# Kernel optimization log

Measured on AMD Instinct MI355X. Metric: run time of the kernel, lower is better.

## Reference

```python
import jax, jax.numpy as jnp
import numpy as np

N_NODES = 50000
N_FEAT = 128
N_EDGES = 800000
HEADS1 = 4
HID1 = 64
HID2 = 128
N_CLASSES = 10
N_GRAPHS = 512
NEG_SLOPE_ATT = 0.2   # GATConv attention leaky relu
NEG_SLOPE_ACT = 0.01  # F.leaky_relu default between layers


def setup_inputs() -> dict:
    key = jax.random.key(0)
    ks = jax.random.split(key, 20)
    s = 0.05
    inp = {
        'x': jax.random.normal(ks[0], (N_NODES, N_FEAT), dtype=jnp.float32),
        'edge_index': jax.random.randint(ks[1], (2, N_EDGES), 0, N_NODES, dtype=jnp.int64),
        'edge_attr': jax.random.normal(ks[2], (N_EDGES, 8), dtype=jnp.float32),
        'batch': jnp.sort(jax.random.randint(ks[3], (N_NODES,), 0, N_GRAPHS, dtype=jnp.int64)),
        # conv1: F -> HID1, heads=4, concat
        'W1': jax.random.normal(ks[4], (N_FEAT, HEADS1 * HID1), dtype=jnp.float32) * s,
        'a_src1': jax.random.normal(ks[5], (HEADS1, HID1), dtype=jnp.float32) * s,
        'a_dst1': jax.random.normal(ks[6], (HEADS1, HID1), dtype=jnp.float32) * s,
        'b1': jnp.zeros((HEADS1 * HID1,), dtype=jnp.float32),
        # conv2: 4*HID1 -> HID2, heads=1
        'W2': jax.random.normal(ks[7], (HEADS1 * HID1, HID2), dtype=jnp.float32) * s,
        'a_src2': jax.random.normal(ks[8], (1, HID2), dtype=jnp.float32) * s,
        'a_dst2': jax.random.normal(ks[9], (1, HID2), dtype=jnp.float32) * s,
        'b2': jnp.zeros((HID2,), dtype=jnp.float32),
        # conv3: HID2 -> N_CLASSES, heads=1
        'W3': jax.random.normal(ks[10], (HID2, N_CLASSES), dtype=jnp.float32) * s,
        'a_src3': jax.random.normal(ks[11], (1, N_CLASSES), dtype=jnp.float32) * s,
        'a_dst3': jax.random.normal(ks[12], (1, N_CLASSES), dtype=jnp.float32) * s,
        'b3': jnp.zeros((N_CLASSES,), dtype=jnp.float32),
    }
    return inp


def gat_conv(x, src, dst, W, a_src, a_dst, b, n_nodes, heads, ch):
    """PyG GATConv (concat=True, add_self_loops already applied in src/dst)."""
    h = (x @ W).reshape(n_nodes, heads, ch)            # [N,H,C]
    al_s = (h * a_src).sum(-1)                          # [N,H]
    al_d = (h * a_dst).sum(-1)                          # [N,H]
    e = jax.nn.leaky_relu(al_s[src] + al_d[dst], NEG_SLOPE_ATT)  # [E,H]
    # segment softmax over incoming edges per destination node
    m = jax.ops.segment_max(e, dst, num_segments=n_nodes)
    ex = jnp.exp(e - m[dst])
    den = jax.ops.segment_sum(ex, dst, num_segments=n_nodes)
    alpha = ex / (den[dst] + 1e-16)                     # [E,H]
    out = jax.ops.segment_sum(h[src] * alpha[..., None], dst, num_segments=n_nodes)
    return out.reshape(n_nodes, heads * ch) + b


def reference(x, edge_index, edge_attr, batch,
              W1, a_src1, a_dst1, b1,
              W2, a_src2, a_dst2, b2,
              W3, a_src3, a_dst3, b3):
    # GATConv adds self-loops by default; edge_attr unused (edge_dim=None)
    loops = jnp.arange(N_NODES, dtype=edge_index.dtype)
    src = jnp.concatenate([edge_index[0], loops])
    dst = jnp.concatenate([edge_index[1], loops])

    h = gat_conv(x, src, dst, W1, a_src1, a_dst1, b1, N_NODES, HEADS1, HID1)
    h = jax.nn.leaky_relu(h, NEG_SLOPE_ACT)
    h = gat_conv(h, src, dst, W2, a_src2, a_dst2, b2, N_NODES, 1, HID2)
    h = jax.nn.leaky_relu(h, NEG_SLOPE_ACT)
    h = gat_conv(h, src, dst, W3, a_src3, a_dst3, b3, N_NODES, 1, N_CLASSES)

    pooled = jax.ops.segment_sum(h, batch, num_segments=N_GRAPHS)  # global_add_pool
    return jax.nn.log_softmax(pooled, axis=1), pooled
```

## Files before the change

### kernel.cpp

```cpp
#include <hip/hip_runtime.h>
#include <math.h>

#define NNODES 50000
#define MPAD   50048
#define NFEAT  128
#define NEDGE  800000
#define ETOT   (NEDGE + NNODES)
#define H1     4
#define O1     256
#define C2     128
#define C3     10
#define NGRAPH 512

#define NBKT   196
#define NBLK1  831
#define EPB    1024
#define SCM    (NBKT * NBLK1)
#define SCB    637

typedef __attribute__((ext_vector_type(8))) short short8;
typedef __attribute__((ext_vector_type(4))) float f32x4;

__device__ __forceinline__ unsigned short f2b(float f) {
  unsigned int u = __float_as_uint(f);
  u += 0x7fffu + ((u >> 16) & 1u);
  return (unsigned short)(u >> 16);
}
__device__ __forceinline__ float b2f(unsigned short u) {
  return __uint_as_float(((unsigned int)u) << 16);
}
__device__ __forceinline__ float readlane_f(float v, int l) {
  return __uint_as_float((unsigned)__builtin_amdgcn_readlane(__float_as_uint(v), l));
}


__global__ void k_prep(const float* __restrict__ W1, const float* __restrict__ as1,
                       const float* __restrict__ ad1,
                       float* __restrict__ was, float* __restrict__ wad) {
  int tid = threadIdx.x;
  int h = tid >> 7, k = tid & 127;
  float s = 0.f, d = 0.f;
  for (int j = 0; j < 64; ++j) {
    float w = W1[(size_t)k * 256 + h * 64 + j];
    s += w * as1[h * 64 + j];
    d += w * ad1[h * 64 + j];
  }
  was[h * 128 + k] = s;
  wad[h * 128 + k] = d;
}

#define NB_CVT 12500

__global__ __launch_bounds__(256) void k_front(
    const int* __restrict__ src_e, const int* __restrict__ dst_e,
    int* __restrict__ hists,
    const float* __restrict__ X, unsigned short* __restrict__ Xb,
    const float* __restrict__ W1,
    const float* __restrict__ was, const float* __restrict__ wad,
    float* __restrict__ als, float* __restrict__ ald,
    unsigned short* __restrict__ W1p,
    const float* __restrict__ W2, unsigned short* __restrict__ W2p,
    const float* __restrict__ W3, unsigned short* __restrict__ W3p) {
  const int b = blockIdx.x;
  const int tid = threadIdx.x;
  if (b < NBLK1) {
    __shared__ int h[NBKT];
    if (tid < NBKT) h[tid] = 0;
    __syncthreads();
    const int base = b * EPB;
#pragma unroll
    for (int r = 0; r < 4; ++r) {
      int e = base + r * 256 + tid;
      if (e < ETOT) {
        int d = (e < NEDGE) ? dst_e[e] : (e - NEDGE);
        atomicAdd(&h[d >> 8], 1);
      }
    }
    __syncthreads();
    if (tid < NBKT) hists[tid * NBLK1 + b] = h[tid];
  } else if (b < NBLK1 + NB_CVT) {
    const int n = (b - NBLK1) * 4 + (tid >> 6);
    const int lane = tid & 63;
    const int k0 = lane * 2;
    float2 xv = *(const float2*)(X + (size_t)n * 128 + k0);
    ushort2 o; o.x = f2b(xv.x); o.y = f2b(xv.y);
    *(ushort2*)(Xb + (size_t)n * 128 + k0) = o;
    float s[4], d[4];
#pragma unroll
    for (int h = 0; h < 4; ++h) {
      float2 wsv = *(const float2*)(was + h * 128 + k0);
      float2 wdv = *(const float2*)(wad + h * 128 + k0);
      s[h] = xv.x * wsv.x + xv.y * wsv.y;
      d[h] = xv.x * wdv.x + xv.y * wdv.y;
    }
#pragma unroll
    for (int m = 1; m < 64; m <<= 1)
#pragma unroll
      for (int h = 0; h < 4; ++h) { s[h] += __shfl_xor(s[h], m); d[h] += __shfl_xor(d[h], m); }
    if (lane == 0) {
#pragma unroll
      for (int h = 0; h < 4; ++h) {
        als[(size_t)n * 4 + h] = s[h];
        ald[(size_t)n * 4 + h] = d[h];
      }
    }
  } else if (b < NBLK1 + NB_CVT + 128) {
    int idx = (b - NBLK1 - NB_CVT) * 256 + tid;
    int h = idx >> 13, r = idx & 8191;
    int j = r & 7, lane = (r >> 3) & 63, t = r >> 9;
    int ks = t & 3, nt = t >> 2;
    int k = ks * 32 + (lane >> 4) * 8 + j;
    int n = nt * 16 + (lane & 15);
    W1p[idx] = f2b(W1[(size_t)k * 256 + h * 64 + n]);
  } else if (b < NBLK1 + NB_CVT + 256) {
    int idx = (b - NBLK1 - NB_CVT - 128) * 256 + tid;
    int j = idx & 7, lane = (idx >> 3) & 63, t = idx >> 9;
    int ks = t % 8, nt = t / 8;
    int k = ks * 32 + (lane >> 4) * 8 + j;
    int n = nt * 16 + (lane & 15);
    W2p[idx] = f2b(W2[(size_t)k * C2 + n]);
  } else {
    int idx = (b - NBLK1 - NB_CVT - 256) * 256 + tid;
    int j = idx & 7, lane = (idx >> 3) & 63, t = idx >> 9;
    int ks = t & 3, nt = t >> 2;
    int k = ks * 32 + (lane >> 4) * 8 + j;
    int n = nt * 16 + (lane & 15);
    W3p[idx] = f2b((n < C3) ? W3[(size_t)k * C3 + n] : 0.f);
  }
}


__global__ __launch_bounds__(256) void k_scanA2(const int* __restrict__ a,
                                                int* __restrict__ bsum) {
  int idx = blockIdx.x * 256 + threadIdx.x;
  int v = (idx < SCM) ? a[idx] : 0;
#pragma unroll
  for (int m = 1; m < 64; m <<= 1) v += __shfl_xor(v, m);
  __shared__ int ws[4];
  int lane = threadIdx.x & 63, wid = threadIdx.x >> 6;
  if (lane == 0) ws[wid] = v;
  __syncthreads();
  if (threadIdx.x == 0) bsum[blockIdx.x] = ws[0] + ws[1] + ws[2] + ws[3];
}

__global__ __launch_bounds__(256) void k_scanMid(int* __restrict__ bsum) {
  __shared__ int ws[4];
  __shared__ int carry_s;
  const int tid = threadIdx.x, lane = tid & 63, wid = tid >> 6;
  if (tid == 0) carry_s = 0;
  __syncthreads();
  for (int base = 0; base < SCB; base += 256) {
    int j = base + tid;
    int v = (j < SCB) ? bsum[j] : 0;
    int s = v;
#pragma unroll
    for (int m = 1; m < 64; m <<= 1) {
      int t = __shfl_up(s, m);
      if (lane >= m) s += t;
    }
    if (lane == 63) ws[wid] = s;
    __syncthreads();
    int woff = 0;
#pragma unroll
    for (int k = 0; k < 4; ++k)
      if (k < wid) woff += ws[k];
    int c = carry_s;
    int tot = ws[0] + ws[1] + ws[2] + ws[3];
    if (j < SCB) bsum[j] = c + woff + s - v;
    __syncthreads();
    if (tid == 0) carry_s = c + tot;
    __syncthreads();
  }
}

__global__ __launch_bounds__(256) void k_scanB2(int* __restrict__ a,
                                                const int* __restrict__ bsum,
                                                int* __restrict__ cb) {
  const int b = blockIdx.x, tid = threadIdx.x;
  const int lane = tid & 63, wid = tid >> 6;
  __shared__ int ws[4];
  int idx = b * 256 + tid;
  int v = (idx < SCM) ? a[idx] : 0;
  int s = v;
#pragma unroll
  for (int m = 1; m < 64; m <<= 1) {
    int t = __shfl_up(s, m);
    if (lane >= m) s += t;
  }
  if (lane == 63) ws[wid] = s;
  __syncthreads();
  int woff = 0;
#pragma unroll
  for (int k = 0; k < 4; ++k)
    if (k < wid) woff += ws[k];
  int excl = bsum[b] + woff + s - v;
  if (idx < SCM) {
    a[idx] = excl;
    if (idx % NBLK1 == 0) cb[idx / NBLK1] = excl;
  }
  if (b == 0 && tid == 0) cb[NBKT] = ETOT;
}


__global__ __launch_bounds__(256) void k_part1(const int* __restrict__ src_e,
                                               const int* __restrict__ dst_e,
                                               const int* __restrict__ offs,
                                               unsigned* __restrict__ coarse) {
  __shared__ int cur[NBKT];
  const int b = blockIdx.x;
  const int tid = threadIdx.x;
  if (tid < NBKT) cur[tid] = offs[tid * NBLK1 + b];
  __syncthreads();
  const int base = b * EPB;
#pragma unroll
  for (int r = 0; r < 4; ++r) {
    int e = base + r * 256 + tid;
    if (e < ETOT) {
      int d, s;
      if (e < NEDGE) { d = dst_e[e]; s = src_e[e]; }
      else           { d = e - NEDGE; s = e - NEDGE; }
      int pos = atomicAdd(&cur[d >> 8], 1);
      coarse[pos] = ((unsigned)d << 16) | (unsigned)s;
    }
  }
}


__global__ __launch_bounds__(256) void k_bucket(const unsigned* __restrict__ coarse,
                                                const int* __restrict__ cb,
                                                int* __restrict__ rowptr,
                                                int* __restrict__ srcs) {
  const int b = blockIdx.x;
  const int tid = threadIdx.x;
  const int lane = tid & 63, wid = tid >> 6;
  const int lo = cb[b], hi = cb[b + 1];
  __shared__ int h[256];
  __shared__ int cur[256];
  __shared__ int ws[4];
  h[tid] = 0;
  __syncthreads();
  for (int i = lo + tid; i < hi; i += 256)
    atomicAdd(&h[(coarse[i] >> 16) & 255], 1);
  __syncthreads();
  int v = h[tid];
  int s = v;
#pragma unroll
  for (int m = 1; m < 64; m <<= 1) {
    int t = __shfl_up(s, m);
    if (lane >= m) s += t;
  }
  if (lane == 63) ws[wid] = s;
  __syncthreads();
  int woff = 0;
#pragma unroll
  for (int k = 0; k < 4; ++k)
    if (k < wid) woff += ws[k];
  int ex = woff + s - v;
  cur[tid] = lo + ex;
  int d = b * 256 + tid;
  if (d < NNODES) rowptr[d] = lo + ex;
  if (b == NBKT - 1 && tid == 0) rowptr[NNODES] = ETOT;
  __syncthreads();
  for (int i = lo + tid; i < hi; i += 256) {
    unsigned c = coarse[i];
    int pos = atomicAdd(&cur[(c >> 16) & 255], 1);
    srcs[pos] = (int)(c & 0xffffu);
  }
}


__global__ __launch_bounds__(512) void k_aggP(const int* __restrict__ rowptr,
                                              const int* __restrict__ srcs,
                                              const unsigned short* __restrict__ Xb,
                                              const float* __restrict__ als,
                                              const float* __restrict__ ald,
                                              unsigned short* __restrict__ P) {
  __shared__ float exs[8][16][4];
  const int wv = threadIdx.x >> 6;
  const int n = blockIdx.x * 8 + wv;
  const int lane = threadIdx.x & 63;
  const int r0 = rowptr[n], r1 = rowptr[n + 1];
  const int e_lane = lane & 15, hh = lane >> 4;
  const float aldv = ald[(size_t)n * 4 + hh];
  const int ch0 = lane * 2;
  float a00 = 0.f, a01 = 0.f, a10 = 0.f, a11 = 0.f;
  float a20 = 0.f, a21 = 0.f, a30 = 0.f, a31 = 0.f;
  float den = 0.f;
  for (int i0 = r0; i0 < r1; i0 += 16) {
    const int take = r1 - i0;
    int sidx = srcs[min(i0 + e_lane, r1 - 1)];
    float ev = als[(size_t)sidx * 4 + hh] + aldv;
    ev = (ev > 0.f) ? ev : 0.2f * ev;
    float exv = (e_lane < take) ? __expf(ev) : 0.f;
    den += exv;
    exs[wv][e_lane][hh] = exv;
    unsigned hv[16];
#pragma unroll
    for (int m = 0; m < 16; ++m) {
      int s = __builtin_amdgcn_readlane(sidx, m);
      hv[m] = *(const unsigned*)(Xb + (size_t)s * 128 + ch0);
    }
#pragma unroll
    for (int m = 0; m < 16; ++m) {
      float4 e4 = *(const float4*)(&exs[wv][m][0]);
      float x0 = __uint_as_float(hv[m] << 16);
      float x1 = __uint_as_float(hv[m] & 0xffff0000u);
      a00 += e4.x * x0; a01 += e4.x * x1;
      a10 += e4.y * x0; a11 += e4.y * x1;
      a20 += e4.z * x0; a21 += e4.z * x1;
      a30 += e4.w * x0; a31 += e4.w * x1;
    }
  }
#pragma unroll
  for (int m = 1; m < 16; m <<= 1) den += __shfl_xor(den, m);
  float acc[4][2] = {{a00,a01},{a10,a11},{a20,a21},{a30,a31}};
#pragma unroll
  for (int h = 0; h < 4; ++h) {
    float rd = 1.f / (readlane_f(den, h * 16) + 1e-16f);
    ushort2 o; o.x = f2b(acc[h][0] * rd); o.y = f2b(acc[h][1] * rd);
    *(ushort2*)(P + ((size_t)n * 4 + h) * 128 + ch0) = o;
  }
}


__global__ __launch_bounds__(256) void k_mmh(const unsigned short* __restrict__ P,
                                             const unsigned short* __restrict__ Wp,
                                             const float* __restrict__ b1,
                                             unsigned short* __restrict__ act1) {
  const int hy = blockIdx.y;
  const int w = threadIdx.x >> 6, lane = threadIdx.x & 63;
  const int arow = blockIdx.x * 64 + w * 16 + (lane & 15);
  const int k0 = (lane >> 4) * 8;
  const unsigned short* Ab = P + ((size_t)arow * 4 + hy) * 128;
  f32x4 acc[4] = {};
#pragma unroll
  for (int ks = 0; ks < 4; ++ks) {
    short8 a = *(const short8*)(Ab + ks * 32 + k0);
    const short8* bp = (const short8*)(Wp + (size_t)hy * 8192) + ks * 64 + lane;
#pragma unroll
    for (int nt = 0; nt < 4; ++nt) {
      short8 b = bp[(size_t)nt * 4 * 64];
      acc[nt] = __builtin_amdgcn_mfma_f32_16x16x32_bf16(a, b, acc[nt], 0, 0, 0);
    }
  }
  const int col = lane & 15;
  const int rbase = blockIdx.x * 64 + w * 16 + (lane >> 4) * 4;
#pragma unroll
  for (int nt = 0; nt < 4; ++nt) {
    int ch = hy * 64 + nt * 16 + col;
    float bb = b1[ch];
#pragma unroll
    for (int j = 0; j < 4; ++j) {
      float v = acc[nt][j] + bb;
      v = (v > 0.f) ? v : 0.01f * v;
      act1[(size_t)(rbase + j) * 256 + ch] = f2b(v);
    }
  }
}


template<int K, int N, int HEADS, int CREAL>
__global__ __launch_bounds__(256) void k_mm(const unsigned short* __restrict__ Xb,
                                            const unsigned short* __restrict__ Wp,
                                            unsigned short* __restrict__ Hout,
                                            const float* __restrict__ a_src,
                                            const float* __restrict__ a_dst,
                                            float* __restrict__ als,
                                            float* __restrict__ ald) {
  constexpr int KS = K / 32, NT = N / 16;
  constexpr int NTH = (NT + HEADS - 1) / HEADS;
  const int w = threadIdx.x >> 6, lane = threadIdx.x & 63;
  const int arow = blockIdx.x * 64 + w * 16 + (lane & 15);
  const int k0 = (lane >> 4) * 8;
  f32x4 acc[NT] = {};
  for (int ks = 0; ks < KS; ++ks) {
    short8 a = *(const short8*)(Xb + (size_t)arow * K + ks * 32 + k0);
    const short8* bp = (const short8*)Wp + (size_t)ks * 64 + lane;
#pragma unroll
    for (int nt = 0; nt < NT; ++nt) {
      short8 b = bp[(size_t)nt * KS * 64];
      acc[nt] = __builtin_amdgcn_mfma_f32_16x16x32_bf16(a, b, acc[nt], 0, 0, 0);
    }
  }
  const int col = lane & 15;
  const int rbase = blockIdx.x * 64 + w * 16 + (lane >> 4) * 4;
#pragma unroll
  for (int nt = 0; nt < NT; ++nt)
#pragma unroll
    for (int j = 0; j < 4; ++j)
      Hout[(size_t)(rbase + j) * N + nt * 16 + col] = f2b(acc[nt][j]);

  float av[NT], dv[NT];
#pragma unroll
  for (int nt = 0; nt < NT; ++nt) {
    int ch = nt * 16 + col;
    av[nt] = (ch < CREAL) ? a_src[ch] : 0.f;
    dv[nt] = (ch < CREAL) ? a_dst[ch] : 0.f;
  }
  float sa[HEADS][4], da[HEADS][4];
#pragma unroll
  for (int h = 0; h < HEADS; ++h)
#pragma unroll
    for (int j = 0; j < 4; ++j) { sa[h][j] = 0.f; da[h][j] = 0.f; }
#pragma unroll
  for (int nt = 0; nt < NT; ++nt) {
    int h = nt / NTH;
#pragma unroll
    for (int j = 0; j < 4; ++j) {
      sa[h][j] += acc[nt][j] * av[nt];
      da[h][j] += acc[nt][j] * dv[nt];
    }
  }
#pragma unroll
  for (int mask = 1; mask < 16; mask <<= 1)
#pragma unroll
    for (int h = 0; h < HEADS; ++h)
#pragma unroll
      for (int j = 0; j < 4; ++j) {
        sa[h][j] += __shfl_xor(sa[h][j], mask);
        da[h][j] += __shfl_xor(da[h][j], mask);
      }
  if (col == 0) {
#pragma unroll
    for (int j = 0; j < 4; ++j)
#pragma unroll
      for (int h = 0; h < HEADS; ++h) {
        als[(size_t)(rbase + j) * HEADS + h] = sa[h][j];
        ald[(size_t)(rbase + j) * HEADS + h] = da[h][j];
      }
  }
}


template<int C, bool ACT>
__global__ __launch_bounds__(512) void k_agg(const int* __restrict__ rowptr,
                                             const int* __restrict__ srcs,
                                             const unsigned short* __restrict__ Hm,
                                             const float* __restrict__ als,
                                             const float* __restrict__ ald,
                                             const float* __restrict__ bias,
                                             unsigned short* __restrict__ outb) {
  const int n = blockIdx.x * 8 + (threadIdx.x >> 6);
  const int lane = threadIdx.x & 63;
  const int r0 = rowptr[n], r1 = rowptr[n + 1];
  const int e_lane = lane & 15;
  const int ch0 = lane * 2;
  const float aldm = ald[n];
  float acc0 = 0.f, acc1 = 0.f, den = 0.f;
  for (int i0 = r0; i0 < r1; i0 += 16) {
    const int take = r1 - i0;
    int sidx = srcs[min(i0 + e_lane, r1 - 1)];
    float ev = als[sidx] + aldm;
    ev = (ev > 0.f) ? ev : 0.2f * ev;
    float exv = (lane < 16 && e_lane < take) ? __expf(ev) : 0.f;
    den += exv;
    unsigned hv[16];
#pragma unroll
    for (int m = 0; m < 16; ++m) {
      int s = __builtin_amdgcn_readlane(sidx, m);
      hv[m] = *(const unsigned*)(Hm + (size_t)s * C + ch0);
    }
#pragma unroll
    for (int m = 0; m < 16; ++m) {
      float ex = readlane_f(exv, m);
      acc0 += ex * __uint_as_float(hv[m] << 16);
      acc1 += ex * __uint_as_float(hv[m] & 0xffff0000u);
    }
  }
#pragma unroll
  for (int mask = 1; mask < 64; mask <<= 1) den += __shfl_xor(den, mask);
  float rden = 1.f / (den + 1e-16f);
  float v0 = acc0 * rden + bias[ch0];
  float v1 = acc1 * rden + bias[ch0 + 1];
  if (ACT) { v0 = (v0 > 0.f) ? v0 : 0.01f * v0; v1 = (v1 > 0.f) ? v1 : 0.01f * v1; }
  ushort2 o; o.x = f2b(v0); o.y = f2b(v1);
  *(ushort2*)(outb + (size_t)n * C + ch0) = o;
}


__global__ __launch_bounds__(512) void k_agg3(const int* __restrict__ rowptr,
                                              const int* __restrict__ srcs,
                                              const unsigned short* __restrict__ Hm,
                                              const float* __restrict__ als,
                                              const float* __restrict__ ald,
                                              const float* __restrict__ bias,
                                              float* __restrict__ pooled,
                                              const int* __restrict__ batch) {
  const int n = blockIdx.x * 8 + (threadIdx.x >> 6);
  const int lane = threadIdx.x & 63;
  const int r0 = rowptr[n], r1 = rowptr[n + 1];
  const int e_lane = lane & 15;
  const float aldm = ald[n];
  float acc = 0.f, den = 0.f;
  for (int i0 = r0; i0 < r1; i0 += 16) {
    const int take = r1 - i0;
    int sidx = srcs[min(i0 + e_lane, r1 - 1)];
    float ev = als[sidx] + aldm;
    ev = (ev > 0.f) ? ev : 0.2f * ev;
    float exv = (lane < 16 && e_lane < take) ? __expf(ev) : 0.f;
    den += exv;
    unsigned short hs[16];
#pragma unroll
    for (int m = 0; m < 16; ++m) {
      int s = __builtin_amdgcn_readlane(sidx, m);
      hs[m] = Hm[(size_t)s * 16 + e_lane];
    }
#pragma unroll
    for (int m = 0; m < 16; ++m) {
      float ex = readlane_f(exv, m);
      acc += ex * b2f(hs[m]);
    }
  }
#pragma unroll
  for (int mask = 1; mask < 64; mask <<= 1) den += __shfl_xor(den, mask);
  if (lane < C3) {
    float val = acc / (den + 1e-16f) + bias[lane];
    atomicAdd(&pooled[(size_t)batch[n] * C3 + lane], val);
  }
}


__global__ void k_lsm(const float* __restrict__ pooled, float* __restrict__ dout) {
  int g = blockIdx.x * 256 + threadIdx.x;
  if (g >= NGRAPH) return;
  float v[C3];
  float mx = -1e30f;
#pragma unroll
  for (int c = 0; c < C3; ++c) { v[c] = pooled[g * C3 + c]; mx = fmaxf(mx, v[c]); }
  float ssum = 0.f;
#pragma unroll
  for (int c = 0; c < C3; ++c) ssum += __expf(v[c] - mx);
  float lse = mx + __logf(ssum);
#pragma unroll
  for (int c = 0; c < C3; ++c) {
    dout[g * C3 + c] = v[c] - lse;
    dout[NGRAPH * C3 + g * C3 + c] = v[c];
  }
}


extern "C" void kernel_launch(void* const* d_in, const int* in_sizes, int n_in,
                              void* d_out, int out_size, void* d_ws, size_t ws_size,
                              hipStream_t stream) {
  (void)in_sizes; (void)n_in; (void)out_size; (void)ws_size;
  const float* x     = (const float*)d_in[0];
  const int*   eix   = (const int*)d_in[1];
  const int*   batch = (const int*)d_in[3];
  const float* W1 = (const float*)d_in[4];
  const float* as1 = (const float*)d_in[5];
  const float* ad1 = (const float*)d_in[6];
  const float* b1 = (const float*)d_in[7];
  const float* W2 = (const float*)d_in[8];
  const float* as2 = (const float*)d_in[9];
  const float* ad2 = (const float*)d_in[10];
  const float* b2 = (const float*)d_in[11];
  const float* W3 = (const float*)d_in[12];
  const float* as3 = (const float*)d_in[13];
  const float* ad3 = (const float*)d_in[14];
  const float* b3 = (const float*)d_in[15];
  const int* src_e = eix;
  const int* dst_e = eix + NEDGE;

  char* ws = (char*)d_ws;
  size_t off = 0;
  auto carve = [&](size_t bytes) -> char* {
    char* p = ws + off;
    off += (bytes + 511) & ~(size_t)511;
    return p;
  };
  int* hists  = (int*)carve((size_t)SCM * 4);
  int* bsum   = (int*)carve((size_t)SCB * 4);
  int* cb     = (int*)carve((size_t)(NBKT + 1) * 4);
  unsigned* coarse = (unsigned*)carve((size_t)ETOT * 4);
  int* rowptr = (int*)carve((size_t)(NNODES + 1) * 4);
  int* srcs   = (int*)carve((size_t)ETOT * 4);
  float* als  = (float*)carve((size_t)MPAD * H1 * 4);
  float* ald  = (float*)carve((size_t)MPAD * H1 * 4);
  float* was  = (float*)carve((size_t)512 * 4);
  float* wad  = (float*)carve((size_t)512 * 4);
  unsigned short* Xb   = (unsigned short*)carve((size_t)MPAD * 128 * 2);
  unsigned short* P    = (unsigned short*)carve((size_t)MPAD * 512 * 2);
  unsigned short* act1 = (unsigned short*)carve((size_t)MPAD * 256 * 2);
  unsigned short* Hb   = (unsigned short*)carve((size_t)MPAD * 128 * 2);
  unsigned short* Xc   = (unsigned short*)carve((size_t)MPAD * 128 * 2);
  unsigned short* H3b  = (unsigned short*)carve((size_t)MPAD * 16 * 2);
  float* pooled = (float*)carve((size_t)NGRAPH * C3 * 4);
  unsigned short* W1p = (unsigned short*)carve((size_t)4 * 8192 * 2);
  unsigned short* W2p = (unsigned short*)carve((size_t)O1 * C2 * 2);
  unsigned short* W3p = (unsigned short*)carve((size_t)C2 * 16 * 2);

  hipMemsetAsync(pooled, 0, (size_t)NGRAPH * C3 * 4, stream);

  k_prep<<<1, 512, 0, stream>>>(W1, as1, ad1, was, wad);
  k_front<<<NBLK1 + NB_CVT + 264, 256, 0, stream>>>(
      src_e, dst_e, hists, x, Xb, W1, was, wad, als, ald, W1p, W2, W2p, W3, W3p);
  k_scanA2<<<SCB, 256, 0, stream>>>(hists, bsum);
  k_scanMid<<<1, 256, 0, stream>>>(bsum);
  k_scanB2<<<SCB, 256, 0, stream>>>(hists, bsum, cb);
  k_part1<<<NBLK1, 256, 0, stream>>>(src_e, dst_e, hists, coarse);
  k_bucket<<<NBKT, 256, 0, stream>>>(coarse, cb, rowptr, srcs);

  const int GB = MPAD / 64;
  const int NB8 = NNODES / 8;

  k_aggP<<<NB8, 512, 0, stream>>>(rowptr, srcs, Xb, als, ald, P);
  k_mmh<<<dim3(GB, 4), 256, 0, stream>>>(P, W1p, b1, act1);

  k_mm<O1, C2, 1, C2><<<GB, 256, 0, stream>>>(act1, W2p, Hb, as2, ad2, als, ald);
  k_agg<C2, true><<<NB8, 512, 0, stream>>>(rowptr, srcs, Hb, als, ald, b2, Xc);

  k_mm<C2, 16, 1, C3><<<GB, 256, 0, stream>>>(Xc, W3p, H3b, as3, ad3, als, ald);
  k_agg3<<<NB8, 512, 0, stream>>>(rowptr, srcs, H3b, als, ald, b3, pooled, batch);

  k_lsm<<<(NGRAPH + 255) / 256, 256, 0, stream>>>(pooled, (float*)d_out);
}
```

Baseline: 228.2 us.

## Use packed FP32 FMAs in aggregation and pack four nodes per wave in layer 3

The layer-1 and layer-2 aggregation inner loops now use v_pk_fma_f32 inline asm, with attention weights staged through shared memory, which roughly halves the FMA instruction count. The layer-3 aggregation kernel previously used only 16 of 64 lanes per wave. It now processes four destination nodes per wave in 16-lane groups, with per-group source indices and weights in LDS, and launches four times fewer blocks. This targets ALU issue cost and idle lanes, at the price of extra LDS traffic and no explicit barrier around the shared-memory reuse within a wave.

```diff
diff --git a/kernel.cpp b/kernel.cpp
--- a/kernel.cpp
+++ b/kernel.cpp
@@ -20,6 +20,7 @@
 
 typedef __attribute__((ext_vector_type(8))) short short8;
 typedef __attribute__((ext_vector_type(4))) float f32x4;
+typedef __attribute__((ext_vector_type(2))) float f32x2;
 
 __device__ __forceinline__ unsigned short f2b(float f) {
   unsigned int u = __float_as_uint(f);
@@ -283,8 +284,7 @@
   const int e_lane = lane & 15, hh = lane >> 4;
   const float aldv = ald[(size_t)n * 4 + hh];
   const int ch0 = lane * 2;
-  float a00 = 0.f, a01 = 0.f, a10 = 0.f, a11 = 0.f;
-  float a20 = 0.f, a21 = 0.f, a30 = 0.f, a31 = 0.f;
+  f32x2 ah0 = {0.f, 0.f}, ah1 = {0.f, 0.f}, ah2 = {0.f, 0.f}, ah3 = {0.f, 0.f};
   float den = 0.f;
   for (int i0 = r0; i0 < r1; i0 += 16) {
     const int take = r1 - i0;
@@ -302,18 +302,24 @@
     }
 #pragma unroll
     for (int m = 0; m < 16; ++m) {
-      float4 e4 = *(const float4*)(&exs[wv][m][0]);
-      float x0 = __uint_as_float(hv[m] << 16);
-      float x1 = __uint_as_float(hv[m] & 0xffff0000u);
-      a00 += e4.x * x0; a01 += e4.x * x1;
-      a10 += e4.y * x0; a11 += e4.y * x1;
-      a20 += e4.z * x0; a21 += e4.z * x1;
-      a30 += e4.w * x0; a31 += e4.w * x1;
+      f32x2 e01 = *(const f32x2*)(&exs[wv][m][0]);
+      f32x2 e23 = *(const f32x2*)(&exs[wv][m][2]);
+      f32x2 x2;
+      x2.x = __uint_as_float(hv[m] << 16);
+      x2.y = __uint_as_float(hv[m] & 0xffff0000u);
+      asm("v_pk_fma_f32 %0, %1, %2, %0 op_sel:[0,0,0] op_sel_hi:[1,0,1]"
+          : "+v"(ah0) : "v"(x2), "v"(e01));
+      asm("v_pk_fma_f32 %0, %1, %2, %0 op_sel:[0,1,0] op_sel_hi:[1,1,1]"
+          : "+v"(ah1) : "v"(x2), "v"(e01));
+      asm("v_pk_fma_f32 %0, %1, %2, %0 op_sel:[0,0,0] op_sel_hi:[1,0,1]"
+          : "+v"(ah2) : "v"(x2), "v"(e23));
+      asm("v_pk_fma_f32 %0, %1, %2, %0 op_sel:[0,1,0] op_sel_hi:[1,1,1]"
+          : "+v"(ah3) : "v"(x2), "v"(e23));
     }
   }
 #pragma unroll
   for (int m = 1; m < 16; m <<= 1) den += __shfl_xor(den, m);
-  float acc[4][2] = {{a00,a01},{a10,a11},{a20,a21},{a30,a31}};
+  float acc[4][2] = {{ah0.x, ah0.y}, {ah1.x, ah1.y}, {ah2.x, ah2.y}, {ah3.x, ah3.y}};
 #pragma unroll
   for (int h = 0; h < 4; ++h) {
     float rd = 1.f / (readlane_f(den, h * 16) + 1e-16f);
@@ -440,13 +446,16 @@
                                              const float* __restrict__ ald,
                                              const float* __restrict__ bias,
                                              unsigned short* __restrict__ outb) {
-  const int n = blockIdx.x * 8 + (threadIdx.x >> 6);
+  __shared__ float exs2[8][16];
+  const int wv = threadIdx.x >> 6;
+  const int n = blockIdx.x * 8 + wv;
   const int lane = threadIdx.x & 63;
   const int r0 = rowptr[n], r1 = rowptr[n + 1];
   const int e_lane = lane & 15;
   const int ch0 = lane * 2;
   const float aldm = ald[n];
-  float acc0 = 0.f, acc1 = 0.f, den = 0.f;
+  f32x2 accP0 = {0.f, 0.f}, accP1 = {0.f, 0.f};
+  float den = 0.f;
   for (int i0 = r0; i0 < r1; i0 += 16) {
     const int take = r1 - i0;
     int sidx = srcs[min(i0 + e_lane, r1 - 1)];
@@ -454,6 +463,7 @@
     ev = (ev > 0.f) ? ev : 0.2f * ev;
     float exv = (lane < 16 && e_lane < take) ? __expf(ev) : 0.f;
     den += exv;
+    if (lane < 16) exs2[wv][lane] = exv;
     unsigned hv[16];
 #pragma unroll
     for (int m = 0; m < 16; ++m) {
@@ -461,14 +471,21 @@
       hv[m] = *(const unsigned*)(Hm + (size_t)s * C + ch0);
     }
 #pragma unroll
-    for (int m = 0; m < 16; ++m) {
-      float ex = readlane_f(exv, m);
-      acc0 += ex * __uint_as_float(hv[m] << 16);
-      acc1 += ex * __uint_as_float(hv[m] & 0xffff0000u);
+    for (int m = 0; m < 16; m += 2) {
+      f32x2 ep = *(const f32x2*)(&exs2[wv][m]);
+      f32x2 xa, xb;
+      xa.x = __uint_as_float(hv[m] << 16);
+      xa.y = __uint_as_float(hv[m + 1] << 16);
+      xb.x = __uint_as_float(hv[m] & 0xffff0000u);
+      xb.y = __uint_as_float(hv[m + 1] & 0xffff0000u);
+      asm("v_pk_fma_f32 %0, %1, %2, %0" : "+v"(accP0) : "v"(ep), "v"(xa));
+      asm("v_pk_fma_f32 %0, %1, %2, %0" : "+v"(accP1) : "v"(ep), "v"(xb));
     }
   }
 #pragma unroll
   for (int mask = 1; mask < 64; mask <<= 1) den += __shfl_xor(den, mask);
+  float acc0 = accP0.x + accP0.y;
+  float acc1 = accP1.x + accP1.y;
   float rden = 1.f / (den + 1e-16f);
   float v0 = acc0 * rden + bias[ch0];
   float v1 = acc1 * rden + bias[ch0 + 1];
@@ -486,36 +503,38 @@
                                               const float* __restrict__ bias,
                                               float* __restrict__ pooled,
                                               const int* __restrict__ batch) {
-  const int n = blockIdx.x * 8 + (threadIdx.x >> 6);
+  __shared__ int   sid_s[8][4][16];
+  __shared__ float exv_s[8][4][16];
+  const int wv = threadIdx.x >> 6;
   const int lane = threadIdx.x & 63;
-  const int r0 = rowptr[n], r1 = rowptr[n + 1];
-  const int e_lane = lane & 15;
-  const float aldm = ald[n];
+  const int g = lane >> 4, el = lane & 15;
+  const int n = blockIdx.x * 32 + wv * 4 + g;
+  const bool valid = n < NNODES;
+  int r0 = 0, r1 = 0;
+  float aldm = 0.f;
+  if (valid) { r0 = rowptr[n]; r1 = rowptr[n + 1]; aldm = ald[n]; }
   float acc = 0.f, den = 0.f;
   for (int i0 = r0; i0 < r1; i0 += 16) {
     const int take = r1 - i0;
-    int sidx = srcs[min(i0 + e_lane, r1 - 1)];
+    int sidx = srcs[min(i0 + el, r1 - 1)];
     float ev = als[sidx] + aldm;
     ev = (ev > 0.f) ? ev : 0.2f * ev;
-    float exv = (lane < 16 && e_lane < take) ? __expf(ev) : 0.f;
+    float exv = (el < take) ? __expf(ev) : 0.f;
     den += exv;
-    unsigned short hs[16];
+    sid_s[wv][g][el] = sidx;
+    exv_s[wv][g][el] = exv;
 #pragma unroll
     for (int m = 0; m < 16; ++m) {
-      int s = __builtin_amdgcn_readlane(sidx, m);
-      hs[m] = Hm[(size_t)s * 16 + e_lane];
-    }
-#pragma unroll
-    for (int m = 0; m < 16; ++m) {
-      float ex = readlane_f(exv, m);
-      acc += ex * b2f(hs[m]);
-    }
-  }
-#pragma unroll
-  for (int mask = 1; mask < 64; mask <<= 1) den += __shfl_xor(den, mask);
-  if (lane < C3) {
-    float val = acc / (den + 1e-16f) + bias[lane];
-    atomicAdd(&pooled[(size_t)batch[n] * C3 + lane], val);
+      int s = sid_s[wv][g][m];
+      float ex = exv_s[wv][g][m];
+      acc += ex * b2f(Hm[(size_t)s * 16 + el]);
+    }
+  }
+#pragma unroll
+  for (int mask = 1; mask < 16; mask <<= 1) den += __shfl_xor(den, mask);
+  if (valid && el < C3) {
+    float val = acc / (den + 1e-16f) + bias[el];
+    atomicAdd(&pooled[(size_t)batch[n] * C3 + el], val);
   }
 }
 
@@ -602,6 +621,7 @@
 
   const int GB = MPAD / 64;
   const int NB8 = NNODES / 8;
+  const int NB32 = (NNODES + 31) / 32;
 
   k_aggP<<<NB8, 512, 0, stream>>>(rowptr, srcs, Xb, als, ald, P);
   k_mmh<<<dim3(GB, 4), 256, 0, stream>>>(P, W1p, b1, act1);
@@ -610,7 +630,7 @@
   k_agg<C2, true><<<NB8, 512, 0, stream>>>(rowptr, srcs, Hb, als, ald, b2, Xc);
 
   k_mm<C2, 16, 1, C3><<<GB, 256, 0, stream>>>(Xc, W3p, H3b, as3, ad3, als, ald);
-  k_agg3<<<NB8, 512, 0, stream>>>(rowptr, srcs, H3b, als, ald, b3, pooled, batch);
+  k_agg3<<<NB32, 512, 0, stream>>>(rowptr, srcs, H3b, als, ald, b3, pooled, batch);
 
   k_lsm<<<(NGRAPH + 255) / 256, 256, 0, stream>>>(pooled, (float*)d_out);
 }
```

Result: no change. 226.4 us (-0.8%).
